# Kernel optimization log

Measured on AMD Instinct MI355X. Metric: run time of the kernel, lower is better.

Reference implementation:

```python
import jax, jax.numpy as jnp
import numpy as np

D = 4096   # number of unique dates (groups)
G = 1024   # stocks per date
N = D * G
TEMPERATURE = 1.0
EPS = 1e-8


def setup_inputs() -> dict:
    key = jax.random.key(0)
    k1, k2 = jax.random.split(key)
    predictions = jax.random.normal(k1, (N, 1), dtype=jnp.float32)
    targets = jax.random.normal(k2, (N, 1), dtype=jnp.float32)
    # sorted date ids, equal-size groups: [0,0,...,0,1,1,...]
    dates = jnp.arange(N, dtype=jnp.int64) // G
    return {"predictions": predictions, "targets": targets, "dates": dates}


def reference(predictions, targets, dates):
    # dates are sorted with equal group size G, so grouping == reshape to [D, G]
    preds = predictions.reshape(D, G)
    tgts = targets.reshape(D, G)

    # per-date softmax over predictions (matches torch.softmax(date_preds/T, dim=0))
    p = jax.nn.softmax(preds / TEMPERATURE, axis=-1)        # [D, G]
    log_pred = jnp.log(p + EPS)                             # torch: log(pred_probs + 1e-8)

    # target ranks: argsort(argsort(targets, descending)) per date
    ranks = jnp.argsort(jnp.argsort(-tgts, axis=-1), axis=-1).astype(preds.dtype)  # [D, G]
    neg_ranks = -ranks / TEMPERATURE
    q = jax.nn.softmax(neg_ranks, axis=-1)                  # target_probs
    log_q = jax.nn.log_softmax(neg_ranks, axis=-1)

    # KL(q || p) summed per date (torch kl_div reduction='sum'), averaged over valid dates
    kl = jnp.sum(q * (log_q - log_pred))
    return kl / D
```

## Files before the change

### kernel.cpp

```cpp
#include <hip/hip_runtime.h>
#include <math.h>

#define D_DATES 4096
#define G_STOCKS 1024
#define KTOP 6
#define EPL 16
#define QD 3
#define WPB 16
#define NBLOCKS (D_DATES / WPB)

#define C_CONST (-1.0406518523f)

static __device__ __forceinline__ unsigned umax(unsigned a, unsigned b) { return a > b ? a : b; }
static __device__ __forceinline__ unsigned umin(unsigned a, unsigned b) { return a < b ? a : b; }
static __device__ __forceinline__ unsigned umin3(unsigned a, unsigned b, unsigned c) { return umin(a, umin(b, c)); }

#define DPPF_MAX(v, ctrl, rm) do { \
    int o_ = __builtin_amdgcn_update_dpp(__float_as_int(v), __float_as_int(v), (ctrl), (rm), 0xF, false); \
    (v) = fmaxf((v), __int_as_float(o_)); } while (0)
#define DPPF_ADD(v, ctrl, rm) do { \
    int o_ = __builtin_amdgcn_update_dpp(0, __float_as_int(v), (ctrl), (rm), 0xF, true); \
    (v) = (v) + __int_as_float(o_); } while (0)

#define MERGE6_STEP(a, ctrl, rm) do { \
    unsigned b0_ = (unsigned)__builtin_amdgcn_update_dpp(0, (int)a[0], (ctrl), (rm), 0xF, true); \
    unsigned b1_ = (unsigned)__builtin_amdgcn_update_dpp(0, (int)a[1], (ctrl), (rm), 0xF, true); \
    unsigned b2_ = (unsigned)__builtin_amdgcn_update_dpp(0, (int)a[2], (ctrl), (rm), 0xF, true); \
    unsigned b3_ = (unsigned)__builtin_amdgcn_update_dpp(0, (int)a[3], (ctrl), (rm), 0xF, true); \
    unsigned b4_ = (unsigned)__builtin_amdgcn_update_dpp(0, (int)a[4], (ctrl), (rm), 0xF, true); \
    unsigned b5_ = (unsigned)__builtin_amdgcn_update_dpp(0, (int)a[5], (ctrl), (rm), 0xF, true); \
    unsigned c0_ = umax(a[0], b0_); \
    unsigned c1_ = umin(umax(a[0], b1_), umax(a[1], b0_)); \
    unsigned c2_ = umin3(umax(a[0], b2_), umax(a[1], b1_), umax(a[2], b0_)); \
    unsigned c3_ = umin(umin(umax(a[0], b3_), umax(a[1], b2_)), umin(umax(a[2], b1_), umax(a[3], b0_))); \
    unsigned c4_ = umin3(umin(umax(a[0], b4_), umax(a[1], b3_)), umin(umax(a[2], b2_), umax(a[3], b1_)), umax(a[4], b0_)); \
    unsigned c5_ = umin3(umin(umax(a[0], b5_), umax(a[1], b4_)), umin(umax(a[2], b3_), umax(a[3], b2_)), umin(umax(a[4], b1_), umax(a[5], b0_))); \
    a[0] = c0_; a[1] = c1_; a[2] = c2_; a[3] = c3_; a[4] = c4_; a[5] = c5_; } while (0)

#define WAVE64_REDUCE(OP, v) do { \
    OP(v, 0x111, 0xF); OP(v, 0x112, 0xF); OP(v, 0x114, 0xF); OP(v, 0x118, 0xF); \
    OP(v, 0x142, 0xA); OP(v, 0x143, 0xC); } while (0)
#define WAVE64_MERGE6(a) do { \
    MERGE6_STEP(a, 0x111, 0xF); MERGE6_STEP(a, 0x112, 0xF); \
    MERGE6_STEP(a, 0x114, 0xF); MERGE6_STEP(a, 0x118, 0xF); \
    MERGE6_STEP(a, 0x142, 0xA); MERGE6_STEP(a, 0x143, 0xC); } while (0)

__global__ __launch_bounds__(1024) void rank_loss_kernel(
    const float* __restrict__ preds,
    const float* __restrict__ tgts,
    float* __restrict__ partials)
{
    const int wave = threadIdx.x >> 6;
    const int lane = threadIdx.x & 63;
    const int row  = blockIdx.x * WPB + wave;

    const float4* __restrict__ xv = (const float4*)(preds + (size_t)row * G_STOCKS);
    const float4* __restrict__ tv = (const float4*)(tgts  + (size_t)row * G_STOCKS);

    float    x[EPL];
    unsigned k[EPL];
#pragma unroll
    for (int j4 = 0; j4 < 4; ++j4) {
        float4 a = xv[lane + 64 * j4];
        float4 b = tv[lane + 64 * j4];
        x[4*j4+0] = a.x; x[4*j4+1] = a.y; x[4*j4+2] = a.z; x[4*j4+3] = a.w;
        float tb[4] = {b.x, b.y, b.z, b.w};
#pragma unroll
        for (int c = 0; c < 4; ++c) {
            unsigned u = __float_as_uint(tb[c]);
            unsigned s = (unsigned)((int)u >> 31);
            k[4*j4+c] = u ^ (s | 0x80000000u);
        }
    }

    float m = x[0];
#pragma unroll
    for (int j = 1; j < EPL; ++j) m = fmaxf(m, x[j]);
    WAVE64_REDUCE(DPPF_MAX, m);
    m = __int_as_float(__builtin_amdgcn_readlane(__float_as_int(m), 63));

    float s = 0.f;
#pragma unroll
    for (int j = 0; j < EPL; ++j) s += __expf(x[j] - m);
    WAVE64_REDUCE(DPPF_ADD, s);
    s = __int_as_float(__builtin_amdgcn_readlane(__float_as_int(s), 63));
    const float inv_s = 1.0f / s;

    unsigned ck[QD]; float cx[QD];
#pragma unroll
    for (int sel = 0; sel < QD; ++sel) {
        unsigned w01 = umax(k[0], k[1]);
        unsigned w23 = umax(k[2], k[3]);
        unsigned w45 = umax(k[4], k[5]);
        unsigned w67 = umax(k[6], k[7]);
        unsigned w89 = umax(k[8], k[9]);
        unsigned wab = umax(k[10], k[11]);
        unsigned wcd = umax(k[12], k[13]);
        unsigned wef = umax(k[14], k[15]);
        unsigned wa0 = umax(w01, w23);
        unsigned wa1 = umax(w45, w67);
        unsigned wa2 = umax(w89, wab);
        unsigned wa3 = umax(wcd, wef);
        const unsigned w = umax(umax(wa0, wa1), umax(wa2, wa3));
        float bx = x[0];
#pragma unroll
        for (int j = 0; j < EPL; ++j) {
            const bool hit = (k[j] == w);
            bx   = hit ? x[j] : bx;
            k[j] = hit ? 0u   : k[j];
        }
        ck[sel] = w; cx[sel] = bx;
    }

    float lp[QD];
#pragma unroll
    for (int j = 0; j < QD; ++j)
        lp[j] = __logf(__expf(cx[j] - m) * inv_s + 1e-8f);

    unsigned a6[6] = { ck[0], ck[1], ck[2], 0u, 0u, 0u };
    WAVE64_MERGE6(a6);
    const unsigned w0 = (unsigned)__builtin_amdgcn_readlane((int)a6[0], 63);
    const unsigned w1 = (unsigned)__builtin_amdgcn_readlane((int)a6[1], 63);
    const unsigned w2 = (unsigned)__builtin_amdgcn_readlane((int)a6[2], 63);
    const unsigned w3 = (unsigned)__builtin_amdgcn_readlane((int)a6[3], 63);
    const unsigned w4 = (unsigned)__builtin_amdgcn_readlane((int)a6[4], 63);
    const unsigned w5 = (unsigned)__builtin_amdgcn_readlane((int)a6[5], 63);

    float kld = 0.f;
#pragma unroll
    for (int j = 0; j < QD; ++j) {
        float c = 0.f;
        c = (ck[j] == w0) ? 0.63212056f : c;
        c = (ck[j] == w1) ? 0.23254416f : c;
        c = (ck[j] == w2) ? 0.08554821f : c;
        c = (ck[j] == w3) ? 0.03147143f : c;
        c = (ck[j] == w4) ? 0.01157769f : c;
        c = (ck[j] == w5) ? 0.00425922f : c;
        kld += c * lp[j];
    }

    WAVE64_REDUCE(DPPF_ADD, kld);

    __shared__ float smw[WPB];
    if (lane == 63) smw[wave] = C_CONST - kld;
    __syncthreads();
    if (threadIdx.x == 0) {
        float p = 0.f;
#pragma unroll
        for (int w = 0; w < WPB; ++w) p += smw[w];
        partials[blockIdx.x] = p;
    }
}

__global__ __launch_bounds__(64) void reduce_partials_kernel(
    const float4* __restrict__ partials,
    float* __restrict__ out)
{
    const float4 v = partials[threadIdx.x];
    float s = (v.x + v.y) + (v.z + v.w);
    WAVE64_REDUCE(DPPF_ADD, s);
    if (threadIdx.x == 63) out[0] = s * (1.0f / (float)D_DATES);
}

extern "C" void kernel_launch(void* const* d_in, const int* in_sizes, int n_in,
                              void* d_out, int out_size, void* d_ws, size_t ws_size,
                              hipStream_t stream) {
    const float* preds = (const float*)d_in[0];
    const float* tgts  = (const float*)d_in[1];
    float* partials = (float*)d_ws;
    float* out      = (float*)d_out;

    rank_loss_kernel<<<NBLOCKS, 1024, 0, stream>>>(preds, tgts, partials);
    reduce_partials_kernel<<<1, 64, 0, stream>>>((const float4*)partials, out);
}
```

Before: 12.68 us.

## Split each row across two waves and merge softmax stats and top-6 via LDS

Each date row is now processed by two waves holding 8 elements per lane instead of one wave with 16. The halves exchange their max/sum and top-6 key lists through shared memory and merge them to get row-wide statistics. This halves per-wave serial work and register pressure and doubles the block count to fill more CUs. In exchange it adds a block barrier, LDS traffic and a larger partial reduction.

```diff
diff --git a/kernel.cpp b/kernel.cpp
--- a/kernel.cpp
+++ b/kernel.cpp
@@ -3,11 +3,10 @@
 
 #define D_DATES 4096
 #define G_STOCKS 1024
-#define KTOP 6
-#define EPL 16
+#define EPL 8
 #define QD 3
-#define WPB 16
-#define NBLOCKS (D_DATES / WPB)
+#define RPB 8
+#define NBLOCKS (D_DATES / RPB)
 
 #define C_CONST (-1.0406518523f)
 
@@ -45,14 +44,16 @@
     MERGE6_STEP(a, 0x114, 0xF); MERGE6_STEP(a, 0x118, 0xF); \
     MERGE6_STEP(a, 0x142, 0xA); MERGE6_STEP(a, 0x143, 0xC); } while (0)
 
-__global__ __launch_bounds__(1024) void rank_loss_kernel(
+__global__ __launch_bounds__(1024, 8) void rank_loss_kernel(
     const float* __restrict__ preds,
     const float* __restrict__ tgts,
     float* __restrict__ partials)
 {
     const int wave = threadIdx.x >> 6;
     const int lane = threadIdx.x & 63;
-    const int row  = blockIdx.x * WPB + wave;
+    const int rib  = wave >> 1;
+    const int half = wave & 1;
+    const int row  = blockIdx.x * RPB + rib;
 
     const float4* __restrict__ xv = (const float4*)(preds + (size_t)row * G_STOCKS);
     const float4* __restrict__ tv = (const float4*)(tgts  + (size_t)row * G_STOCKS);
@@ -60,9 +61,10 @@
     float    x[EPL];
     unsigned k[EPL];
 #pragma unroll
-    for (int j4 = 0; j4 < 4; ++j4) {
-        float4 a = xv[lane + 64 * j4];
-        float4 b = tv[lane + 64 * j4];
+    for (int j4 = 0; j4 < 2; ++j4) {
+        const int fi = half * 128 + 64 * j4 + lane;
+        float4 a = xv[fi];
+        float4 b = tv[fi];
         x[4*j4+0] = a.x; x[4*j4+1] = a.y; x[4*j4+2] = a.z; x[4*j4+3] = a.w;
         float tb[4] = {b.x, b.y, b.z, b.w};
 #pragma unroll
@@ -84,7 +86,6 @@
     for (int j = 0; j < EPL; ++j) s += __expf(x[j] - m);
     WAVE64_REDUCE(DPPF_ADD, s);
     s = __int_as_float(__builtin_amdgcn_readlane(__float_as_int(s), 63));
-    const float inv_s = 1.0f / s;
 
     unsigned ck[QD]; float cx[QD];
 #pragma unroll
@@ -93,15 +94,7 @@
         unsigned w23 = umax(k[2], k[3]);
         unsigned w45 = umax(k[4], k[5]);
         unsigned w67 = umax(k[6], k[7]);
-        unsigned w89 = umax(k[8], k[9]);
-        unsigned wab = umax(k[10], k[11]);
-        unsigned wcd = umax(k[12], k[13]);
-        unsigned wef = umax(k[14], k[15]);
-        unsigned wa0 = umax(w01, w23);
-        unsigned wa1 = umax(w45, w67);
-        unsigned wa2 = umax(w89, wab);
-        unsigned wa3 = umax(wcd, wef);
-        const unsigned w = umax(umax(wa0, wa1), umax(wa2, wa3));
+        const unsigned w = umax(umax(w01, w23), umax(w45, w67));
         float bx = x[0];
 #pragma unroll
         for (int j = 0; j < EPL; ++j) {
@@ -112,42 +105,59 @@
         ck[sel] = w; cx[sel] = bx;
     }
 
+    unsigned a6[6] = { ck[0], ck[1], ck[2], 0u, 0u, 0u };
+    WAVE64_MERGE6(a6);
+
+    __shared__ float2   stats[2 * RPB];
+    __shared__ unsigned lists[2 * RPB][6];
+    __shared__ float    smw[2 * RPB];
+    if (lane == 63) {
+        stats[wave] = make_float2(m, s);
+#pragma unroll
+        for (int j = 0; j < 6; ++j) lists[wave][j] = a6[j];
+    }
+    __syncthreads();
+
+    const float2 po = stats[wave ^ 1];
+    const float  M  = fmaxf(m, po.x);
+    const float  S  = s * __expf(m - M) + po.y * __expf(po.x - M);
+    const float  inv_S = 1.0f / S;
+
+    unsigned A[6], B[6], W[6];
+#pragma unroll
+    for (int j = 0; j < 6; ++j) { A[j] = lists[wave][j]; B[j] = lists[wave ^ 1][j]; }
+    W[0] = umax(A[0], B[0]);
+    W[1] = umin(umax(A[0], B[1]), umax(A[1], B[0]));
+    W[2] = umin3(umax(A[0], B[2]), umax(A[1], B[1]), umax(A[2], B[0]));
+    W[3] = umin(umin(umax(A[0], B[3]), umax(A[1], B[2])), umin(umax(A[2], B[1]), umax(A[3], B[0])));
+    W[4] = umin3(umin(umax(A[0], B[4]), umax(A[1], B[3])), umin(umax(A[2], B[2]), umax(A[3], B[1])), umax(A[4], B[0]));
+    W[5] = umin3(umin(umax(A[0], B[5]), umax(A[1], B[4])), umin(umax(A[2], B[3]), umax(A[3], B[2])), umin(umax(A[4], B[1]), umax(A[5], B[0])));
+
     float lp[QD];
 #pragma unroll
     for (int j = 0; j < QD; ++j)
-        lp[j] = __logf(__expf(cx[j] - m) * inv_s + 1e-8f);
-
-    unsigned a6[6] = { ck[0], ck[1], ck[2], 0u, 0u, 0u };
-    WAVE64_MERGE6(a6);
-    const unsigned w0 = (unsigned)__builtin_amdgcn_readlane((int)a6[0], 63);
-    const unsigned w1 = (unsigned)__builtin_amdgcn_readlane((int)a6[1], 63);
-    const unsigned w2 = (unsigned)__builtin_amdgcn_readlane((int)a6[2], 63);
-    const unsigned w3 = (unsigned)__builtin_amdgcn_readlane((int)a6[3], 63);
-    const unsigned w4 = (unsigned)__builtin_amdgcn_readlane((int)a6[4], 63);
-    const unsigned w5 = (unsigned)__builtin_amdgcn_readlane((int)a6[5], 63);
+        lp[j] = __logf(__expf(cx[j] - M) * inv_S + 1e-8f);
 
     float kld = 0.f;
 #pragma unroll
     for (int j = 0; j < QD; ++j) {
         float c = 0.f;
-        c = (ck[j] == w0) ? 0.63212056f : c;
-        c = (ck[j] == w1) ? 0.23254416f : c;
-        c = (ck[j] == w2) ? 0.08554821f : c;
-        c = (ck[j] == w3) ? 0.03147143f : c;
-        c = (ck[j] == w4) ? 0.01157769f : c;
-        c = (ck[j] == w5) ? 0.00425922f : c;
+        c = (ck[j] == W[0]) ? 0.63212056f : c;
+        c = (ck[j] == W[1]) ? 0.23254416f : c;
+        c = (ck[j] == W[2]) ? 0.08554821f : c;
+        c = (ck[j] == W[3]) ? 0.03147143f : c;
+        c = (ck[j] == W[4]) ? 0.01157769f : c;
+        c = (ck[j] == W[5]) ? 0.00425922f : c;
         kld += c * lp[j];
     }
 
     WAVE64_REDUCE(DPPF_ADD, kld);
-
-    __shared__ float smw[WPB];
-    if (lane == 63) smw[wave] = C_CONST - kld;
+    if (lane == 63) smw[wave] = 0.5f * C_CONST - kld;
     __syncthreads();
     if (threadIdx.x == 0) {
         float p = 0.f;
 #pragma unroll
-        for (int w = 0; w < WPB; ++w) p += smw[w];
+        for (int w = 0; w < 2 * RPB; ++w) p += smw[w];
         partials[blockIdx.x] = p;
     }
 }
@@ -156,8 +166,9 @@
     const float4* __restrict__ partials,
     float* __restrict__ out)
 {
-    const float4 v = partials[threadIdx.x];
-    float s = (v.x + v.y) + (v.z + v.w);
+    const float4 v0 = partials[threadIdx.x];
+    const float4 v1 = partials[threadIdx.x + 64];
+    float s = ((v0.x + v0.y) + (v0.z + v0.w)) + ((v1.x + v1.y) + (v1.z + v1.w));
     WAVE64_REDUCE(DPPF_ADD, s);
     if (threadIdx.x == 63) out[0] = s * (1.0f / (float)D_DATES);
 }
```

Result: slower. 15.06 us (+18.8%).
